# Kernel tuning notes

Hardware: AMD Instinct MI355X
Metric: run time of the kernel (lower is better)

## Reference

```python
import jax, jax.numpy as jnp
import numpy as np

N_NODES = 100000
N_EDGES = 3200000
IN_DIM, HID_DIM, OUT_DIM = 512, 32, 16


def spmm(rows, cols, vals, dense):
    # out[r] = sum_{e: rows[e]==r} vals[e] * dense[cols[e]]  == adj @ dense (COO)
    gathered = vals[:, None] * dense[cols]          # [E, D]
    return jax.ops.segment_sum(gathered, rows, num_segments=N_NODES)


def gcn_layer(x, adj_rows, adj_cols, adj_vals, W):
    support = x @ W                                  # dense mm [N, out]
    return spmm(adj_rows, adj_cols, adj_vals, support)


def setup_inputs() -> dict:
    key = jax.random.key(0)
    ks = jax.random.split(key, 8)
    x = jax.random.normal(ks[0], (N_NODES, IN_DIM), dtype=jnp.float32)
    adj_rows = jax.random.randint(ks[1], (N_EDGES,), 0, N_NODES, dtype=jnp.int32)
    adj_cols = jax.random.randint(ks[2], (N_EDGES,), 0, N_NODES, dtype=jnp.int32)
    adj_vals = jax.random.uniform(ks[3], (N_EDGES,), dtype=jnp.float32)
    W1 = jax.random.normal(ks[4], (IN_DIM, HID_DIM), dtype=jnp.float32)
    W2 = jax.random.normal(ks[5], (HID_DIM, OUT_DIM), dtype=jnp.float32)
    W3 = jax.random.normal(ks[6], (OUT_DIM, HID_DIM), dtype=jnp.float32)
    W4 = jax.random.normal(ks[7], (HID_DIM, IN_DIM), dtype=jnp.float32)
    return {"x": x, "adj_rows": adj_rows, "adj_cols": adj_cols,
            "adj_vals": adj_vals, "W1": W1, "W2": W2, "W3": W3, "W4": W4}


def reference(x, adj_rows, adj_cols, adj_vals, W1, W2, W3, W4):
    encoded1 = gcn_layer(x, adj_rows, adj_cols, adj_vals, W1)        # [N, 32]
    encoded2 = gcn_layer(encoded1, adj_rows, adj_cols, adj_vals, W2) # [N, 16]
    decoded1 = gcn_layer(encoded2, adj_rows, adj_cols, adj_vals, W3) # [N, 32]
    decoded2 = gcn_layer(decoded1, adj_rows, adj_cols, adj_vals, W4) # [N, 512]
    return (decoded2, encoded2)
```

## Files before the change

kernel.cpp:

```cpp
#include <hip/hip_runtime.h>
#include <hip/hip_bf16.h>


#define N_NODES 100000
#define N_EDGES 3200000
#define RPB_LOG 7
#define RPB (1 << RPB_LOG)
#define NB ((N_NODES + RPB - 1) / RPB)
#define CHUNK 16384
#define NCHUNK ((N_EDGES + CHUNK - 1) / CHUNK)
#define EPT (CHUNK / 512)

typedef __attribute__((ext_vector_type(4))) float f32x4;
typedef __attribute__((ext_vector_type(8))) short s16x8;
typedef __attribute__((ext_vector_type(4))) unsigned short u16x4;
typedef __attribute__((ext_vector_type(4))) int i32x4;

static __device__ inline s16x8 cvt8(const float4& lo, const float4& hi) {
  unsigned p0, p1, p2, p3;
  asm("v_cvt_pk_bf16_f32 %0, %1, %2" : "=v"(p0) : "v"(lo.x), "v"(lo.y));
  asm("v_cvt_pk_bf16_f32 %0, %1, %2" : "=v"(p1) : "v"(lo.z), "v"(lo.w));
  asm("v_cvt_pk_bf16_f32 %0, %1, %2" : "=v"(p2) : "v"(hi.x), "v"(hi.y));
  asm("v_cvt_pk_bf16_f32 %0, %1, %2" : "=v"(p3) : "v"(hi.z), "v"(hi.w));
  i32x4 pi = {(int)p0, (int)p1, (int)p2, (int)p3};
  return __builtin_bit_cast(s16x8, pi);
}

static __device__ inline unsigned pk2(float a, float b) {
  unsigned p;
  asm("v_cvt_pk_bf16_f32 %0, %1, %2" : "=v"(p) : "v"(a), "v"(b));
  return p;
}
static __device__ inline float b2f(unsigned short u) {
  return __uint_as_float(((unsigned)u) << 16);
}

__global__ __launch_bounds__(256) void wconv12_kernel(
    const float* __restrict__ W1, const float* __restrict__ W2,
    uint4* __restrict__ Wfrag) {
  int s = blockIdx.x * 256 + threadIdx.x;
  if (s >= 1024) return;
  int lane = s & 63, kt = s >> 6;
  int n = lane & 15;
  int kb = kt * 32 + (lane >> 4) * 8;
  unsigned p[4];
#pragma unroll
  for (int i = 0; i < 4; ++i) {
    float lo = 0.f, hi = 0.f;
#pragma unroll
    for (int m = 0; m < 32; ++m) {
      float w2 = W2[m * 16 + n];
      lo += W1[(kb + 2 * i) * 32 + m] * w2;
      hi += W1[(kb + 2 * i + 1) * 32 + m] * w2;
    }
    p[i] = pk2(lo, hi);
  }
  Wfrag[s] = make_uint4(p[0], p[1], p[2], p[3]);
}

__global__ __launch_bounds__(256) void mm1_kernel(
    const float* __restrict__ x, const uint4* __restrict__ Wfrag,
    unsigned short* __restrict__ out) {
  const int t = threadIdx.x;
  const int lane = t & 63;
  const int w = t >> 6;
  const int rbase = blockIdx.x * 128 + w * 32;
  const int lrow = lane & 15;
  const int kg = lane >> 4;

  int r0c = rbase + lrow;       if (r0c > N_NODES - 1) r0c = N_NODES - 1;
  int r1c = rbase + 16 + lrow;  if (r1c > N_NODES - 1) r1c = N_NODES - 1;
  const float* xp0 = x + (size_t)r0c * 512 + kg * 8;
  const float* xp1 = x + (size_t)r1c * 512 + kg * 8;
  const s16x8* Wf = (const s16x8*)Wfrag;

  f32x4 acc0 = {0.f, 0.f, 0.f, 0.f}, acc1 = {0.f, 0.f, 0.f, 0.f};

#pragma unroll 4
  for (int kt = 0; kt < 16; ++kt) {
    float4 a0lo = *(const float4*)(xp0 + kt * 32);
    float4 a0hi = *(const float4*)(xp0 + kt * 32 + 4);
    float4 a1lo = *(const float4*)(xp1 + kt * 32);
    float4 a1hi = *(const float4*)(xp1 + kt * 32 + 4);
    s16x8 b = Wf[kt * 64 + lane];
    s16x8 a0 = cvt8(a0lo, a0hi);
    s16x8 a1 = cvt8(a1lo, a1hi);
    acc0 = __builtin_amdgcn_mfma_f32_16x16x32_bf16(a0, b, acc0, 0, 0, 0);
    acc1 = __builtin_amdgcn_mfma_f32_16x16x32_bf16(a1, b, acc1, 0, 0, 0);
  }

  const int col = lane & 15;
#pragma unroll
  for (int reg = 0; reg < 4; ++reg) {
    int r0 = rbase + kg * 4 + reg;
    if (r0 < N_NODES)
      out[(size_t)r0 * 16 + col] = (unsigned short)(pk2(acc0[reg], acc0[reg]) & 0xFFFF);
    int r1 = rbase + 16 + kg * 4 + reg;
    if (r1 < N_NODES)
      out[(size_t)r1 * 16 + col] = (unsigned short)(pk2(acc1[reg], acc1[reg]) & 0xFFFF);
  }
}

__global__ __launch_bounds__(512) void localsort_kernel(
    const int* __restrict__ rows, const int* __restrict__ cols,
    const float* __restrict__ vals, int2* __restrict__ cv_loc,
    int* __restrict__ ofs, int* __restrict__ gcnt) {
  __shared__ int lcnt[NB];
  __shared__ int lofs[NB + 1];
  __shared__ int ssum[512];
  const int c = blockIdx.x, t = threadIdx.x;
  const int c0 = c * CHUNK, c1 = min(c0 + CHUNK, N_EDGES);

  for (int i = t; i < NB; i += 512) lcnt[i] = 0;
  __syncthreads();

  int rr[EPT];
#pragma unroll
  for (int u = 0; u < EPT; ++u) {
    int e = c0 + t + u * 512;
    rr[u] = (e < c1) ? rows[e] : -1;
    if (rr[u] >= 0) atomicAdd(&lcnt[rr[u] >> RPB_LOG], 1);
  }
  __syncthreads();

  int v0 = (2 * t < NB) ? lcnt[2 * t] : 0;
  int v1 = (2 * t + 1 < NB) ? lcnt[2 * t + 1] : 0;
  if (v0) atomicAdd(&gcnt[2 * t], v0);
  if (v1) atomicAdd(&gcnt[2 * t + 1], v1);
  ssum[t] = v0 + v1;
  __syncthreads();
  for (int off = 1; off < 512; off <<= 1) {
    int xv = (t >= off) ? ssum[t - off] : 0;
    __syncthreads();
    ssum[t] += xv;
    __syncthreads();
  }
  int excl = (t == 0) ? 0 : ssum[t - 1];
  if (2 * t < NB) lofs[2 * t] = excl;
  if (2 * t + 1 < NB) lofs[2 * t + 1] = excl + v0;
  if (t == 511) lofs[NB] = ssum[511];
  __syncthreads();

  for (int i = t; i <= NB; i += 512) ofs[c * (NB + 1) + i] = lofs[i];
  for (int i = t; i < NB; i += 512) lcnt[i] = 0;
  __syncthreads();

#pragma unroll
  for (int u = 0; u < EPT; ++u) {
    int r = rr[u];
    if (r >= 0) {
      int e = c0 + t + u * 512;
      int b = r >> RPB_LOG;
      int rank = atomicAdd(&lcnt[b], 1);
      cv_loc[c0 + lofs[b] + rank] =
          make_int2(((r & (RPB - 1)) << 17) | cols[e], __float_as_int(vals[e]));
    }
  }
}

__global__ __launch_bounds__(256) void refine5_kernel(
    const int* __restrict__ ofs, const int* __restrict__ gcnt,
    const int2* __restrict__ cv_loc, unsigned* __restrict__ cv_csr,
    int* __restrict__ row_ptr) {
  __shared__ int gs[NCHUNK];
  __shared__ int q[NCHUNK + 1];
  __shared__ int sq[256];
  __shared__ int rcnt[RPB];
  __shared__ int rbase[RPB];
  __shared__ int bstart_s;
  const int b = blockIdx.x, t = threadIdx.x;

  int part = 0;
  for (int i = t; i < b; i += 256) part += gcnt[i];
  sq[t] = part;
  __syncthreads();
  for (int off = 128; off > 0; off >>= 1) {
    if (t < off) sq[t] += sq[t + off];
    __syncthreads();
  }
  if (t == 0) bstart_s = sq[0];
  __syncthreads();

  int cnt_t = 0;
  if (t < NCHUNK) {
    int g0 = ofs[t * (NB + 1) + b];
    int g1 = ofs[t * (NB + 1) + b + 1];
    gs[t] = t * CHUNK + g0;
    cnt_t = g1 - g0;
  }
  sq[t] = cnt_t;
  __syncthreads();
  for (int off = 1; off < 256; off <<= 1) {
    int v = (t >= off) ? sq[t - off] : 0;
    __syncthreads();
    sq[t] += v;
    __syncthreads();
  }
  if (t < NCHUNK) q[t] = sq[t] - cnt_t;
  if (t == 0) q[NCHUNK] = sq[255];
  if (t < RPB) rcnt[t] = 0;
  __syncthreads();
  const int Q = q[NCHUNK];

  int lo = 0;
  for (int i = t; i < Q; i += 256) {
    while (q[lo + 1] <= i) ++lo;
    int2 e = cv_loc[gs[lo] + (i - q[lo])];
    atomicAdd(&rcnt[e.x >> 17], 1);
  }
  __syncthreads();

  int rv = (t < RPB) ? rcnt[t] : 0;
  sq[t] = rv;
  __syncthreads();
  for (int off = 1; off < RPB; off <<= 1) {
    int v = (t >= off && t < RPB) ? sq[t - off] : 0;
    __syncthreads();
    if (t < RPB) sq[t] += v;
    __syncthreads();
  }
  if (t < RPB) {
    int base = bstart_s + sq[t] - rv;
    rbase[t] = base;
    int gr = (b << RPB_LOG) + t;
    if (gr < N_NODES) row_ptr[gr] = base;
    rcnt[t] = 0;
  }
  if (b == 0 && t == 0) row_ptr[N_NODES] = N_EDGES;
  __syncthreads();

  lo = 0;
  for (int i = t; i < Q; i += 256) {
    while (q[lo + 1] <= i) ++lo;
    int2 e = cv_loc[gs[lo] + (i - q[lo])];
    int rl = e.x >> 17;
    int rank = atomicAdd(&rcnt[rl], 1);
    float v = __int_as_float(e.y);
    unsigned vb = pk2(v, v);
    cv_csr[rbase[rl] + rank] =
        ((unsigned)(e.x & 0x1FFFF) << 15) | (vb & 0x7FFF);
  }
}

template <int OM>
__global__ __launch_bounds__(256) void spmm_b16_kernel(
    const int* __restrict__ rp, const unsigned* __restrict__ colval,
    const unsigned short* __restrict__ in, unsigned short* __restrict__ outb,
    float* __restrict__ outf) {
  const int t = threadIdx.x;
  const int r = blockIdx.x * 32 + (t >> 3);
  const int q = t & 3;
  const int hh = (t >> 2) & 1;
  const int k0 = rp[r], k1 = rp[r + 1];
  const int len0 = (k1 - k0 + 1) >> 1;
  int k = k0 + hh * len0;
  const int ke = hh ? k1 : (k0 + len0);
  float a0 = 0.f, a1 = 0.f, a2 = 0.f, a3 = 0.f;

  for (; k + 7 < ke; k += 8) {
    unsigned cv[8];
#pragma unroll
    for (int u = 0; u < 8; ++u) cv[u] = colval[k + u];
    u16x4 g[8];
#pragma unroll
    for (int u = 0; u < 8; ++u)
      g[u] = *(const u16x4*)(in + (size_t)(cv[u] >> 15) * 16 + q * 4);
#pragma unroll
    for (int u = 0; u < 8; ++u) {
      float v = __uint_as_float((cv[u] & 0x7FFF) << 16);
      a0 += v * b2f(g[u][0]);
      a1 += v * b2f(g[u][1]);
      a2 += v * b2f(g[u][2]);
      a3 += v * b2f(g[u][3]);
    }
  }
  for (; k + 3 < ke; k += 4) {
    unsigned cv[4];
#pragma unroll
    for (int u = 0; u < 4; ++u) cv[u] = colval[k + u];
    u16x4 g[4];
#pragma unroll
    for (int u = 0; u < 4; ++u)
      g[u] = *(const u16x4*)(in + (size_t)(cv[u] >> 15) * 16 + q * 4);
#pragma unroll
    for (int u = 0; u < 4; ++u) {
      float v = __uint_as_float((cv[u] & 0x7FFF) << 16);
      a0 += v * b2f(g[u][0]);
      a1 += v * b2f(g[u][1]);
      a2 += v * b2f(g[u][2]);
      a3 += v * b2f(g[u][3]);
    }
  }
  for (; k < ke; ++k) {
    unsigned cv = colval[k];
    u16x4 g = *(const u16x4*)(in + (size_t)(cv >> 15) * 16 + q * 4);
    float v = __uint_as_float((cv & 0x7FFF) << 16);
    a0 += v * b2f(g[0]); a1 += v * b2f(g[1]);
    a2 += v * b2f(g[2]); a3 += v * b2f(g[3]);
  }

  a0 += __shfl_xor(a0, 4);
  a1 += __shfl_xor(a1, 4);
  a2 += __shfl_xor(a2, 4);
  a3 += __shfl_xor(a3, 4);

  if (hh == 0) {
    uint2 pk = make_uint2(pk2(a0, a1), pk2(a2, a3));
    *(uint2*)(outb + (size_t)r * 16 + q * 4) = pk;
    if (OM == 1)
      *(float4*)(outf + (size_t)r * 16 + q * 4) = make_float4(a0, a1, a2, a3);
  }
}

__global__ __launch_bounds__(256) void spmm_dec_kernel(
    const int* __restrict__ rp, const unsigned* __restrict__ colval,
    const unsigned short* __restrict__ in, const float* __restrict__ W3,
    const float* __restrict__ W4, float* __restrict__ out) {
  __shared__ float t3s[32][20];
  const int t = threadIdx.x;
  const int r0 = blockIdx.x * 32;
  const int lr = t >> 3;
  const int q = t & 3;
  const int hh = (t >> 2) & 1;
  const int r = r0 + lr;

  float wa[16], wb[16];
#pragma unroll
  for (int kk = 0; kk < 16; ++kk) { wa[kk] = 0.f; wb[kk] = 0.f; }
#pragma unroll
  for (int m = 0; m < 32; ++m) {
    float w4A = W4[m * 512 + t];
    float w4B = W4[m * 512 + t + 256];
#pragma unroll
    for (int kk = 0; kk < 16; ++kk) {
      float w3 = W3[kk * 32 + m];
      wa[kk] += w3 * w4A;
      wb[kk] += w3 * w4B;
    }
  }

  const int k0 = rp[r], k1 = rp[r + 1];
  const int len0 = (k1 - k0 + 1) >> 1;
  int k = k0 + hh * len0;
  const int ke = hh ? k1 : (k0 + len0);
  float a0 = 0.f, a1 = 0.f, a2 = 0.f, a3 = 0.f;
  for (; k + 7 < ke; k += 8) {
    unsigned cv[8];
#pragma unroll
    for (int u = 0; u < 8; ++u) cv[u] = colval[k + u];
    u16x4 g[8];
#pragma unroll
    for (int u = 0; u < 8; ++u)
      g[u] = *(const u16x4*)(in + (size_t)(cv[u] >> 15) * 16 + q * 4);
#pragma unroll
    for (int u = 0; u < 8; ++u) {
      float v = __uint_as_float((cv[u] & 0x7FFF) << 16);
      a0 += v * b2f(g[u][0]);
      a1 += v * b2f(g[u][1]);
      a2 += v * b2f(g[u][2]);
      a3 += v * b2f(g[u][3]);
    }
  }
  for (; k + 3 < ke; k += 4) {
    unsigned cv[4];
#pragma unroll
    for (int u = 0; u < 4; ++u) cv[u] = colval[k + u];
    u16x4 g[4];
#pragma unroll
    for (int u = 0; u < 4; ++u)
      g[u] = *(const u16x4*)(in + (size_t)(cv[u] >> 15) * 16 + q * 4);
#pragma unroll
    for (int u = 0; u < 4; ++u) {
      float v = __uint_as_float((cv[u] & 0x7FFF) << 16);
      a0 += v * b2f(g[u][0]);
      a1 += v * b2f(g[u][1]);
      a2 += v * b2f(g[u][2]);
      a3 += v * b2f(g[u][3]);
    }
  }
  for (; k < ke; ++k) {
    unsigned cv = colval[k];
    u16x4 g = *(const u16x4*)(in + (size_t)(cv >> 15) * 16 + q * 4);
    float v = __uint_as_float((cv & 0x7FFF) << 16);
    a0 += v * b2f(g[0]); a1 += v * b2f(g[1]);
    a2 += v * b2f(g[2]); a3 += v * b2f(g[3]);
  }
  a0 += __shfl_xor(a0, 4);
  a1 += __shfl_xor(a1, 4);
  a2 += __shfl_xor(a2, 4);
  a3 += __shfl_xor(a3, 4);
  if (hh == 0) {
    t3s[lr][q * 4 + 0] = a0;
    t3s[lr][q * 4 + 1] = a1;
    t3s[lr][q * 4 + 2] = a2;
    t3s[lr][q * 4 + 3] = a3;
  }
  __syncthreads();

  for (int rr = 0; rr < 32; ++rr) {
    float4 c0 = *(const float4*)&t3s[rr][0];
    float4 c1 = *(const float4*)&t3s[rr][4];
    float4 c2 = *(const float4*)&t3s[rr][8];
    float4 c3 = *(const float4*)&t3s[rr][12];
    float sa = c0.x * wa[0] + c0.y * wa[1] + c0.z * wa[2] + c0.w * wa[3]
             + c1.x * wa[4] + c1.y * wa[5] + c1.z * wa[6] + c1.w * wa[7]
             + c2.x * wa[8] + c2.y * wa[9] + c2.z * wa[10] + c2.w * wa[11]
             + c3.x * wa[12] + c3.y * wa[13] + c3.z * wa[14] + c3.w * wa[15];
    float sb = c0.x * wb[0] + c0.y * wb[1] + c0.z * wb[2] + c0.w * wb[3]
             + c1.x * wb[4] + c1.y * wb[5] + c1.z * wb[6] + c1.w * wb[7]
             + c2.x * wb[8] + c2.y * wb[9] + c2.z * wb[10] + c2.w * wb[11]
             + c3.x * wb[12] + c3.y * wb[13] + c3.z * wb[14] + c3.w * wb[15];
    float* o = out + (size_t)(r0 + rr) * 512;
    o[t] = sa;
    o[t + 256] = sb;
  }
}

extern "C" void kernel_launch(void* const* d_in, const int* in_sizes, int n_in,
                              void* d_out, int out_size, void* d_ws, size_t ws_size,
                              hipStream_t stream) {
  const float* x     = (const float*)d_in[0];
  const int*   arows = (const int*)d_in[1];
  const int*   acols = (const int*)d_in[2];
  const float* avals = (const float*)d_in[3];
  const float* W1    = (const float*)d_in[4];
  const float* W2    = (const float*)d_in[5];
  const float* W3    = (const float*)d_in[6];
  const float* W4    = (const float*)d_in[7];

  float* out = (float*)d_out;
  float* dec = out;
  float* enc = out + (size_t)N_NODES * 512;

  unsigned short* bh  = (unsigned short*)d_ws;
  unsigned short* bu  = bh + (size_t)N_NODES * 16;
  unsigned short* be  = bu + (size_t)N_NODES * 16;
  unsigned* cv_csr  = (unsigned*)(be + (size_t)N_NODES * 16);
  int*      row_ptr = (int*)(cv_csr + N_EDGES);

  int2*  cv_loc = (int2*)dec;
  uint4* Wfrag  = (uint4*)(cv_loc + N_EDGES);
  int*   ofs    = (int*)(Wfrag + 1024);
  int*   gcnt   = ofs + NCHUNK * (NB + 1);

  hipMemsetAsync(gcnt, 0, NB * sizeof(int), stream);
  wconv12_kernel<<<4, 256, 0, stream>>>(W1, W2, Wfrag);
  localsort_kernel<<<NCHUNK, 512, 0, stream>>>(arows, acols, avals, cv_loc, ofs, gcnt);
  refine5_kernel<<<NB, 256, 0, stream>>>(ofs, gcnt, cv_loc, cv_csr, row_ptr);

  const int spGrid = N_NODES / 32;
  mm1_kernel<<<(N_NODES + 127) / 128, 256, 0, stream>>>(x, Wfrag, bh);
  spmm_b16_kernel<0><<<spGrid, 256, 0, stream>>>(row_ptr, cv_csr, bh, bu, nullptr);
  spmm_b16_kernel<1><<<spGrid, 256, 0, stream>>>(row_ptr, cv_csr, bu, be, enc);
  spmm_b16_kernel<0><<<spGrid, 256, 0, stream>>>(row_ptr, cv_csr, be, bh, nullptr);
  spmm_dec_kernel<<<spGrid, 256, 0, stream>>>(row_ptr, cv_csr, bh, W3, W4, dec);
}
```

Baseline: 365.1 us.

## Split K across waves in mm1 and shrink intermediate edge records

mm1 now has each block cover 64 rows, with two waves splitting the 512-wide K dimension in halves and reducing partial sums through shared memory. This doubles the grid and the number of outstanding loads on the memory-bound x read. Separately, localsort now writes a 1-byte local-row array plus a packed 32-bit col/bf16 value instead of 8-byte int2 records. This cuts the bytes refine reads and writes, at the cost of an extra scattered byte store and moving the bf16 conversion earlier.

```diff
diff --git a/kernel.cpp b/kernel.cpp
--- a/kernel.cpp
+++ b/kernel.cpp
@@ -61,28 +61,31 @@
 __global__ __launch_bounds__(256) void mm1_kernel(
     const float* __restrict__ x, const uint4* __restrict__ Wfrag,
     unsigned short* __restrict__ out) {
+  __shared__ float part[2][32][17];
   const int t = threadIdx.x;
   const int lane = t & 63;
   const int w = t >> 6;
-  const int rbase = blockIdx.x * 128 + w * 32;
+  const int tile = w & 1;
+  const int kh = w >> 1;
+  const int rbase = blockIdx.x * 64 + tile * 32;
   const int lrow = lane & 15;
   const int kg = lane >> 4;
 
   int r0c = rbase + lrow;       if (r0c > N_NODES - 1) r0c = N_NODES - 1;
   int r1c = rbase + 16 + lrow;  if (r1c > N_NODES - 1) r1c = N_NODES - 1;
-  const float* xp0 = x + (size_t)r0c * 512 + kg * 8;
-  const float* xp1 = x + (size_t)r1c * 512 + kg * 8;
+  const float* xp0 = x + (size_t)r0c * 512 + kh * 256 + kg * 8;
+  const float* xp1 = x + (size_t)r1c * 512 + kh * 256 + kg * 8;
   const s16x8* Wf = (const s16x8*)Wfrag;
 
   f32x4 acc0 = {0.f, 0.f, 0.f, 0.f}, acc1 = {0.f, 0.f, 0.f, 0.f};
 
 #pragma unroll 4
-  for (int kt = 0; kt < 16; ++kt) {
+  for (int kt = 0; kt < 8; ++kt) {
     float4 a0lo = *(const float4*)(xp0 + kt * 32);
     float4 a0hi = *(const float4*)(xp0 + kt * 32 + 4);
     float4 a1lo = *(const float4*)(xp1 + kt * 32);
     float4 a1hi = *(const float4*)(xp1 + kt * 32 + 4);
-    s16x8 b = Wf[kt * 64 + lane];
+    s16x8 b = Wf[(kh * 8 + kt) * 64 + lane];
     s16x8 a0 = cvt8(a0lo, a0hi);
     s16x8 a1 = cvt8(a1lo, a1hi);
     acc0 = __builtin_amdgcn_mfma_f32_16x16x32_bf16(a0, b, acc0, 0, 0, 0);
@@ -90,21 +93,38 @@
   }
 
   const int col = lane & 15;
-#pragma unroll
-  for (int reg = 0; reg < 4; ++reg) {
-    int r0 = rbase + kg * 4 + reg;
-    if (r0 < N_NODES)
-      out[(size_t)r0 * 16 + col] = (unsigned short)(pk2(acc0[reg], acc0[reg]) & 0xFFFF);
-    int r1 = rbase + 16 + kg * 4 + reg;
-    if (r1 < N_NODES)
-      out[(size_t)r1 * 16 + col] = (unsigned short)(pk2(acc1[reg], acc1[reg]) & 0xFFFF);
+  if (kh == 1) {
+#pragma unroll
+    for (int reg = 0; reg < 4; ++reg) {
+      part[tile][kg * 4 + reg][col] = acc0[reg];
+      part[tile][16 + kg * 4 + reg][col] = acc1[reg];
+    }
+  }
+  __syncthreads();
+  if (kh == 0) {
+#pragma unroll
+    for (int reg = 0; reg < 4; ++reg) {
+      int l0 = kg * 4 + reg;
+      int r0 = rbase + l0;
+      if (r0 < N_NODES) {
+        float v = acc0[reg] + part[tile][l0][col];
+        out[(size_t)r0 * 16 + col] = (unsigned short)(pk2(v, v) & 0xFFFF);
+      }
+      int l1 = 16 + kg * 4 + reg;
+      int r1 = rbase + l1;
+      if (r1 < N_NODES) {
+        float v = acc1[reg] + part[tile][l1][col];
+        out[(size_t)r1 * 16 + col] = (unsigned short)(pk2(v, v) & 0xFFFF);
+      }
+    }
   }
 }
 
 __global__ __launch_bounds__(512) void localsort_kernel(
     const int* __restrict__ rows, const int* __restrict__ cols,
-    const float* __restrict__ vals, int2* __restrict__ cv_loc,
-    int* __restrict__ ofs, int* __restrict__ gcnt) {
+    const float* __restrict__ vals, unsigned char* __restrict__ rl_loc,
+    unsigned* __restrict__ cv32_loc, int* __restrict__ ofs,
+    int* __restrict__ gcnt) {
   __shared__ int lcnt[NB];
   __shared__ int lofs[NB + 1];
   __shared__ int ssum[512];
@@ -152,15 +172,18 @@
       int e = c0 + t + u * 512;
       int b = r >> RPB_LOG;
       int rank = atomicAdd(&lcnt[b], 1);
-      cv_loc[c0 + lofs[b] + rank] =
-          make_int2(((r & (RPB - 1)) << 17) | cols[e], __float_as_int(vals[e]));
-    }
-  }
-}
-
-__global__ __launch_bounds__(256) void refine5_kernel(
+      int pos = c0 + lofs[b] + rank;
+      float v = vals[e];
+      rl_loc[pos] = (unsigned char)(r & (RPB - 1));
+      cv32_loc[pos] = ((unsigned)cols[e] << 15) | (pk2(v, v) & 0x7FFF);
+    }
+  }
+}
+
+__global__ __launch_bounds__(256) void refine6_kernel(
     const int* __restrict__ ofs, const int* __restrict__ gcnt,
-    const int2* __restrict__ cv_loc, unsigned* __restrict__ cv_csr,
+    const unsigned char* __restrict__ rl_loc,
+    const unsigned* __restrict__ cv32_loc, unsigned* __restrict__ cv_csr,
     int* __restrict__ row_ptr) {
   __shared__ int gs[NCHUNK];
   __shared__ int q[NCHUNK + 1];
@@ -205,8 +228,7 @@
   int lo = 0;
   for (int i = t; i < Q; i += 256) {
     while (q[lo + 1] <= i) ++lo;
-    int2 e = cv_loc[gs[lo] + (i - q[lo])];
-    atomicAdd(&rcnt[e.x >> 17], 1);
+    atomicAdd(&rcnt[rl_loc[gs[lo] + (i - q[lo])]], 1);
   }
   __syncthreads();
 
@@ -232,13 +254,10 @@
   lo = 0;
   for (int i = t; i < Q; i += 256) {
     while (q[lo + 1] <= i) ++lo;
-    int2 e = cv_loc[gs[lo] + (i - q[lo])];
-    int rl = e.x >> 17;
+    int idx = gs[lo] + (i - q[lo]);
+    int rl = rl_loc[idx];
     int rank = atomicAdd(&rcnt[rl], 1);
-    float v = __int_as_float(e.y);
-    unsigned vb = pk2(v, v);
-    cv_csr[rbase[rl] + rank] =
-        ((unsigned)(e.x & 0x1FFFF) << 15) | (vb & 0x7FFF);
+    cv_csr[rbase[rl] + rank] = cv32_loc[idx];
   }
 }
 
@@ -438,18 +457,21 @@
   unsigned* cv_csr  = (unsigned*)(be + (size_t)N_NODES * 16);
   int*      row_ptr = (int*)(cv_csr + N_EDGES);
 
-  int2*  cv_loc = (int2*)dec;
-  uint4* Wfrag  = (uint4*)(cv_loc + N_EDGES);
-  int*   ofs    = (int*)(Wfrag + 1024);
-  int*   gcnt   = ofs + NCHUNK * (NB + 1);
+  unsigned char* rl_loc   = (unsigned char*)dec;
+  unsigned*      cv32_loc = (unsigned*)(rl_loc + ((N_EDGES + 15) & ~15));
+  uint4*         Wfrag    = (uint4*)(cv32_loc + N_EDGES);
+  int*           ofs      = (int*)(Wfrag + 1024);
+  int*           gcnt     = ofs + NCHUNK * (NB + 1);
 
   hipMemsetAsync(gcnt, 0, NB * sizeof(int), stream);
   wconv12_kernel<<<4, 256, 0, stream>>>(W1, W2, Wfrag);
-  localsort_kernel<<<NCHUNK, 512, 0, stream>>>(arows, acols, avals, cv_loc, ofs, gcnt);
-  refine5_kernel<<<NB, 256, 0, stream>>>(ofs, gcnt, cv_loc, cv_csr, row_ptr);
+  localsort_kernel<<<NCHUNK, 512, 0, stream>>>(arows, acols, avals, rl_loc,
+                                               cv32_loc, ofs, gcnt);
+  refine6_kernel<<<NB, 256, 0, stream>>>(ofs, gcnt, rl_loc, cv32_loc,
+                                         cv_csr, row_ptr);
 
   const int spGrid = N_NODES / 32;
-  mm1_kernel<<<(N_NODES + 127) / 128, 256, 0, stream>>>(x, Wfrag, bh);
+  mm1_kernel<<<(N_NODES + 63) / 64, 256, 0, stream>>>(x, Wfrag, bh);
   spmm_b16_kernel<0><<<spGrid, 256, 0, stream>>>(row_ptr, cv_csr, bh, bu, nullptr);
   spmm_b16_kernel<1><<<spGrid, 256, 0, stream>>>(row_ptr, cv_csr, bu, be, enc);
   spmm_b16_kernel<0><<<spGrid, 256, 0, stream>>>(row_ptr, cv_csr, be, bh, nullptr);
```

Result: slower. 398.9 us (+9.3%).
